# Kernel tuning notes

Measured on AMD Instinct MI355X. Metric: run time of the kernel, lower is better.

## Reference

```python
import jax, jax.numpy as jnp
import numpy as np

N = 8192       # nodes per graph
E = 262144     # edges per graph (avg degree 32)
H = 8          # attention heads
C = 128        # hidden dim per head (H*C = 1024 to match Linear(1024,128))
IN = 128       # input feature dim
NEG_SLOPE = 0.2


def _gat_conv(x, edge_index, W, att_src, att_dst, bias):
    """PyG GATConv (concat=True, add_self_loops=True, shared lin for src/dst)."""
    n = x.shape[0]
    loop = jnp.arange(n, dtype=edge_index.dtype)
    src = jnp.concatenate([edge_index[0], loop])  # [E+N]
    dst = jnp.concatenate([edge_index[1], loop])
    h = (x @ W).reshape(n, H, C)                         # [N,H,C]
    a_src = jnp.sum(h * att_src, axis=-1)                # [N,H]
    a_dst = jnp.sum(h * att_dst, axis=-1)                # [N,H]
    e = jax.nn.leaky_relu(a_src[src] + a_dst[dst], NEG_SLOPE)   # [E+N,H]
    m = jax.ops.segment_max(e, dst, num_segments=n)      # per-dst max for stability
    ex = jnp.exp(e - m[dst])
    den = jax.ops.segment_sum(ex, dst, num_segments=n)
    alpha = ex / den[dst]                                # [E+N,H] neighborhood softmax
    out = jax.ops.segment_sum(h[src] * alpha[:, :, None], dst, num_segments=n)
    return out.reshape(n, H * C) + bias                  # [N, H*C]


def setup_inputs() -> dict:
    key = jax.random.key(0)
    ks = jax.random.split(key, 12)
    s = 0.05  # keep activations in a sane range
    return {
        "x1": jax.random.normal(ks[0], (N, IN), jnp.float32),
        "edge_index1": jax.random.randint(ks[1], (2, E), 0, N, dtype=jnp.int64),
        "W1": jax.random.normal(ks[2], (IN, H * C), jnp.float32) * s,
        "att_src1": jax.random.normal(ks[3], (H, C), jnp.float32) * s,
        "att_dst1": jax.random.normal(ks[4], (H, C), jnp.float32) * s,
        "b1": jnp.zeros((H * C,), jnp.float32),
        "x2": jax.random.normal(ks[5], (N, IN), jnp.float32),
        "edge_index2": jax.random.randint(ks[6], (2, E), 0, N, dtype=jnp.int64),
        "W2": jax.random.normal(ks[7], (IN, H * C), jnp.float32) * s,
        "att_src2": jax.random.normal(ks[8], (H, C), jnp.float32) * s,
        "att_dst2": jax.random.normal(ks[9], (H, C), jnp.float32) * s,
        "b2": jnp.zeros((H * C,), jnp.float32),
        "Wl": jax.random.normal(ks[10], (H * C, 128), jnp.float32) * s,
        "bl": jnp.zeros((128,), jnp.float32),
    }


def reference(x1, edge_index1, W1, att_src1, att_dst1, b1,
              x2, edge_index2, W2, att_src2, att_dst2, b2, Wl, bl):
    emb1 = _gat_conv(x1, edge_index1, W1, att_src1, att_dst1, b1)  # [N1,1024]
    emb2 = _gat_conv(x2, edge_index2, W2, att_src2, att_dst2, b2)  # [N2,1024]
    scores = emb1 @ emb2.T                                          # [N1,N2]
    w1 = jax.nn.softmax(scores, axis=1)
    w2 = jax.nn.softmax(scores, axis=0)
    cross1 = (w2 @ emb2) @ Wl + bl      # [N1,128]
    cross2 = (w1.T @ emb1) @ Wl + bl    # [N2,128]
    return (jnp.mean(cross1, axis=0), jnp.mean(cross2, axis=0))
```

## Files before the change

### kernel.cpp

```cpp
#include <hip/hip_runtime.h>


#define NN 8192
#define EE 262144
#define NEG 0.2f

#define BKT 128
#define RNG (NN / BKT)
#define CAP 2560
#define EB  128
#define CHK (EE / EB)

#define U_CNT   0
#define U_G     (U_CNT + 4*BKT)
#define U_MEMB  (U_G + 2048)
#define U_ZEND  (U_MEMB + 2048)
#define U_U     (U_ZEND)
#define U_ASRC  (U_U + 2*2048)
#define U_ADST  (U_ASRC + 2*NN*8)
#define U_PR    (U_ADST + 2*NN*8)
#define U_WACC  (U_PR + 2*NN*16)
#define U_BIND  (U_WACC + 2*NN*8)
#define U_BINS  (U_BIND + 2*BKT*CAP)
#define ZERO_BYTES ((size_t)U_ZEND * 4)

__global__ __launch_bounds__(256) void k_u(
    const float* __restrict__ W1, const float* __restrict__ as1, const float* __restrict__ ad1,
    const float* __restrict__ W2, const float* __restrict__ as2, const float* __restrict__ ad2,
    float* __restrict__ u) {
  int b = blockIdx.x;
  int graph = b >> 4, sd = (b >> 3) & 1, head = b & 7;
  const float* W = graph ? W2 : W1;
  const float* att = graph ? (sd ? ad2 : as2) : (sd ? ad1 : as1);
  int w = threadIdx.x >> 6, lane = threadIdx.x & 63;
  float2 av = ((const float2*)(att + head * 128))[lane];
  float* uo = u + graph * 2048 + sd * 1024 + head * 128;
#pragma unroll 4
  for (int k = w; k < 128; k += 4) {
    float2 wv = ((const float2*)(W + (size_t)k * 1024 + head * 128))[lane];
    float p = av.x * wv.x + av.y * wv.y;
    p += __shfl_xor(p, 1);  p += __shfl_xor(p, 2);  p += __shfl_xor(p, 4);
    p += __shfl_xor(p, 8);  p += __shfl_xor(p, 16); p += __shfl_xor(p, 32);
    if (lane == 0) uo[k] = p;
  }
}

__global__ __launch_bounds__(256) void k_a(
    const float* __restrict__ x1, const float* __restrict__ x2,
    const float* __restrict__ u, float* __restrict__ asrc, float* __restrict__ adst) {
  int graph = blockIdx.y;
  const float* x = graph ? x2 : x1;
  const float* ug = u + graph * 2048;
  __shared__ float xs[64][129];
  __shared__ float us[16][128];
  int t = threadIdx.x;
  for (int i = t; i < 2048; i += 256) us[i >> 7][i & 127] = ug[i];
  int n0 = blockIdx.x * 64;
  const float* xb = x + (size_t)n0 * 128;
  for (int i = t; i < 64 * 128; i += 256) xs[i >> 7][i & 127] = xb[i];
  __syncthreads();
  int nl = t & 63;
  int j0 = (t >> 6) * 4;
  float a0 = 0.f, a1 = 0.f, a2 = 0.f, a3 = 0.f;
#pragma unroll 4
  for (int k = 0; k < 128; ++k) {
    float xv = xs[nl][k];
    a0 += xv * us[j0 + 0][k];
    a1 += xv * us[j0 + 1][k];
    a2 += xv * us[j0 + 2][k];
    a3 += xv * us[j0 + 3][k];
  }
  int n = n0 + nl;
  float* outp = (j0 < 8) ? (asrc + graph * (NN * 8) + n * 8 + j0)
                         : (adst + graph * (NN * 8) + n * 8 + (j0 - 8));
  outp[0] = a0; outp[1] = a1; outp[2] = a2; outp[3] = a3;
}

__global__ __launch_bounds__(512) void k_bin(
    const int* __restrict__ ei1, const int* __restrict__ ei2,
    int* __restrict__ cnt, int* __restrict__ binD, int* __restrict__ binS) {
  int g = blockIdx.y;
  const int* ei = g ? ei2 : ei1;
  __shared__ int hD[BKT], hS[BKT], scD[BKT], scS[BKT];
  __shared__ int cD[BKT], cS[BKT], bD[BKT], bS[BKT];
  __shared__ int ldsD[CHK], ldsS[CHK];
  __shared__ unsigned char kbAD[CHK], kbAS[CHK];
  int t = threadIdx.x;
  if (t < BKT) { hD[t] = 0; cD[t] = 0; }
  else if (t < 2 * BKT) { int i = t - BKT; hS[i] = 0; cS[i] = 0; }
  __syncthreads();
  int e0 = blockIdx.x * CHK;
  int sv[4], dv[4];
#pragma unroll
  for (int k = 0; k < 4; ++k) {
    sv[k] = ei[e0 + t + k * 512];
    dv[k] = ei[EE + e0 + t + k * 512];
    atomicAdd(&hD[dv[k] >> 6], 1);
    atomicAdd(&hS[sv[k] >> 6], 1);
  }
  __syncthreads();
  if (t < BKT) { scD[t] = hD[t]; bD[t] = atomicAdd(cnt + (2 * g + 0) * BKT + t, hD[t]); }
  else if (t < 2 * BKT) { int i = t - BKT; scS[i] = hS[i]; bS[i] = atomicAdd(cnt + (2 * g + 1) * BKT + i, hS[i]); }
  __syncthreads();
  for (int o = 1; o < BKT; o <<= 1) {
    int v = 0;
    if (t < BKT) { if (t >= o) v = scD[t - o]; }
    else if (t < 2 * BKT) { int i = t - BKT; if (i >= o) v = scS[i - o]; }
    __syncthreads();
    if (t < BKT) scD[t] += v;
    else if (t < 2 * BKT) scS[t - BKT] += v;
    __syncthreads();
  }
#pragma unroll
  for (int k = 0; k < 4; ++k) {
    int kb = dv[k] >> 6;
    int pos = (scD[kb] - hD[kb]) + atomicAdd(&cD[kb], 1);
    ldsD[pos] = (sv[k] << 6) | (dv[k] & 63);
    kbAD[pos] = (unsigned char)kb;
    kb = sv[k] >> 6;
    pos = (scS[kb] - hS[kb]) + atomicAdd(&cS[kb], 1);
    ldsS[pos] = (dv[k] << 6) | (sv[k] & 63);
    kbAS[pos] = (unsigned char)kb;
  }
  __syncthreads();
  int* bdg = binD + (size_t)g * BKT * CAP;
  int* bsg = binS + (size_t)g * BKT * CAP;
#pragma unroll
  for (int k = 0; k < 4; ++k) {
    int i = t + k * 512;
    int kb = kbAD[i];
    bdg[kb * CAP + bD[kb] + (i - (scD[kb] - hD[kb]))] = ldsD[i];
    kb = kbAS[i];
    bsg[kb * CAP + bS[kb] + (i - (scS[kb] - hS[kb]))] = ldsS[i];
  }
}

__global__ __launch_bounds__(512) void k_den_red(
    const int* __restrict__ cnt, const int* __restrict__ binD,
    const float* __restrict__ asrc, const float* __restrict__ adst,
    float* __restrict__ pr) {
  int g = blockIdx.y, b = blockIdx.x;
  int lo = b * RNG;
  const float* as = asrc + g * (NN * 8);
  const float* ad = adst + g * (NN * 8);
  float2* prg = (float2*)pr + (size_t)g * (NN * 8);
  __shared__ float den[8][RNG];
  __shared__ float adsts[8][RNG];
  int t = threadIdx.x;
  {
    int dl = t & 63, h = t >> 6;
    float avv = ad[(lo + dl) * 8 + h];
    float v = as[(lo + dl) * 8 + h] + avv;
    v = v > 0.f ? v : NEG * v;
    adsts[h][dl] = avv;
    den[h][dl] = __expf(v);
  }
  __syncthreads();
  int n = cnt[(2 * g + 0) * BKT + b];
  const int* recs = binD + (size_t)g * BKT * CAP + b * CAP;
  for (int base = 0; base < n; base += 2048) {
    int rv[4]; bool ok[4]; float4 q0[4], q1[4];
#pragma unroll
    for (int k = 0; k < 4; ++k) {
      int i = base + k * 512 + t;
      ok[k] = i < n;
      rv[k] = ok[k] ? recs[i] : 0;
    }
#pragma unroll
    for (int k = 0; k < 4; ++k) {
      const float4* p = (const float4*)(as + (size_t)(rv[k] >> 6) * 8);
      if (ok[k]) { q0[k] = p[0]; q1[k] = p[1]; }
    }
#pragma unroll
    for (int k = 0; k < 4; ++k) {
      if (ok[k]) {
        int dl = rv[k] & 63;
        float e[8] = {q0[k].x, q0[k].y, q0[k].z, q0[k].w,
                      q1[k].x, q1[k].y, q1[k].z, q1[k].w};
#pragma unroll
        for (int h = 0; h < 8; ++h) {
          float v = e[h] + adsts[h][dl];
          v = v > 0.f ? v : NEG * v;
          atomicAdd(&den[h][dl], __expf(v));
        }
      }
    }
  }
  __syncthreads();
  {
    int dl = t >> 3, h = t & 7;
    prg[lo * 8 + t] = make_float2(adsts[h][dl], 1.0f / den[h][dl]);
  }
}

__global__ __launch_bounds__(512) void k_wacc_red(
    const int* __restrict__ cnt, const int* __restrict__ binS,
    const float* __restrict__ asrc, const float* __restrict__ pr,
    float* __restrict__ wacc) {
  int g = blockIdx.y, b = blockIdx.x;
  int lo = b * RNG;
  const float* as = asrc + g * (NN * 8);
  const float2* prg = (const float2*)pr + (size_t)g * (NN * 8);
  __shared__ float wv[8][RNG];
  __shared__ float asrcs[8][RNG];
  int t = threadIdx.x;
  {
    int sl = t & 63, h = t >> 6;
    float sva = as[(lo + sl) * 8 + h];
    float2 f2 = prg[(lo + sl) * 8 + h];
    float v = sva + f2.x;
    v = v > 0.f ? v : NEG * v;
    asrcs[h][sl] = sva;
    wv[h][sl] = __expf(v) * f2.y;
  }
  __syncthreads();
  int n = cnt[(2 * g + 1) * BKT + b];
  const int* recs = binS + (size_t)g * BKT * CAP + b * CAP;
  for (int base = 0; base < n; base += 2048) {
    int rv[4]; bool ok[4]; float4 q0[4], q1[4], q2[4], q3[4];
#pragma unroll
    for (int k = 0; k < 4; ++k) {
      int i = base + k * 512 + t;
      ok[k] = i < n;
      rv[k] = ok[k] ? recs[i] : 0;
    }
#pragma unroll
    for (int k = 0; k < 4; ++k) {
      const float4* p = (const float4*)(prg + (size_t)(rv[k] >> 6) * 8);
      if (ok[k]) { q0[k] = p[0]; q1[k] = p[1]; q2[k] = p[2]; q3[k] = p[3]; }
    }
#pragma unroll
    for (int k = 0; k < 4; ++k) {
      if (ok[k]) {
        int sl = rv[k] & 63;
        float a[8] = {q0[k].x, q0[k].z, q1[k].x, q1[k].z,
                      q2[k].x, q2[k].z, q3[k].x, q3[k].z};
        float r[8] = {q0[k].y, q0[k].w, q1[k].y, q1[k].w,
                      q2[k].y, q2[k].w, q3[k].y, q3[k].w};
#pragma unroll
        for (int h = 0; h < 8; ++h) {
          float v = asrcs[h][sl] + a[h];
          v = v > 0.f ? v : NEG * v;
          atomicAdd(&wv[h][sl], __expf(v) * r[h]);
        }
      }
    }
  }
  __syncthreads();
  {
    int sl = t >> 3, h = t & 7;
    wacc[g * (NN * 8) + lo * 8 + t] = wv[h][sl];
  }
}

#define GCHUNK 256
__global__ __launch_bounds__(256) void k_gred(
    const float* __restrict__ x1, const float* __restrict__ x2,
    const float* __restrict__ wacc, float* __restrict__ g) {
  int graph = blockIdx.y;
  const float* x = graph ? x2 : x1;
  const float* w = wacc + graph * (NN * 8);
  float* gg = g + graph * 1024;
  int t = threadIdx.x;
  int k = t & 127;
  int h0 = (t >> 7) * 4;
  int n0 = blockIdx.x * GCHUNK;
  float a0 = 0.f, a1 = 0.f, a2 = 0.f, a3 = 0.f;
#pragma unroll 4
  for (int n = n0; n < n0 + GCHUNK; ++n) {
    float xv = x[(size_t)n * 128 + k];
    float4 wv4 = *(const float4*)(w + (size_t)n * 8 + h0);
    a0 += xv * wv4.x; a1 += xv * wv4.y; a2 += xv * wv4.z; a3 += xv * wv4.w;
  }
  atomicAdd(gg + (h0 + 0) * 128 + k, a0);
  atomicAdd(gg + (h0 + 1) * 128 + k, a1);
  atomicAdd(gg + (h0 + 2) * 128 + k, a2);
  atomicAdd(gg + (h0 + 3) * 128 + k, a3);
}

__global__ __launch_bounds__(256) void k_memb(
    const float* __restrict__ W1, const float* __restrict__ W2,
    const float* __restrict__ b1, const float* __restrict__ b2,
    const float* __restrict__ g, float* __restrict__ memb) {
  int graph = blockIdx.z;
  int kc = blockIdx.y;
  const float* W = graph ? W2 : W1;
  const float* b = graph ? b2 : b1;
  int e = blockIdx.x * 256 + threadIdx.x;
  int head = e >> 7;
  const float* gr = g + graph * 1024 + head * 128;
  float s = 0.f;
#pragma unroll
  for (int k = kc * 16; k < kc * 16 + 16; ++k) s += gr[k] * W[(size_t)k * 1024 + e];
  s *= (1.0f / (float)NN);
  if (kc == 0) s += b[e];
  atomicAdd(memb + graph * 1024 + e, s);
}

__global__ __launch_bounds__(256) void k_out(
    const float* __restrict__ memb, const float* __restrict__ Wl,
    const float* __restrict__ bl, float* __restrict__ out) {
  int t = threadIdx.x;
  int j = t & 127;
  int k0 = blockIdx.x * 32;
  const float* m = (t < 128) ? (memb + 1024) : memb;
  float s = 0.f;
#pragma unroll
  for (int k = k0; k < k0 + 32; ++k) s += m[k] * Wl[(size_t)k * 128 + j];
  if (blockIdx.x == 0) s += bl[j];
  atomicAdd(out + t, s);
}

extern "C" void kernel_launch(void* const* d_in, const int* in_sizes, int n_in,
                              void* d_out, int out_size, void* d_ws, size_t ws_size,
                              hipStream_t stream) {
  const float* x1  = (const float*)d_in[0];
  const int*   ei1 = (const int*)d_in[1];
  const float* W1  = (const float*)d_in[2];
  const float* as1 = (const float*)d_in[3];
  const float* ad1 = (const float*)d_in[4];
  const float* b1  = (const float*)d_in[5];
  const float* x2  = (const float*)d_in[6];
  const int*   ei2 = (const int*)d_in[7];
  const float* W2  = (const float*)d_in[8];
  const float* as2 = (const float*)d_in[9];
  const float* ad2 = (const float*)d_in[10];
  const float* b2  = (const float*)d_in[11];
  const float* Wl  = (const float*)d_in[12];
  const float* bl  = (const float*)d_in[13];
  float* out = (float*)d_out;

  int*   cnt  = (int*)d_ws + U_CNT;
  float* g    = (float*)d_ws + U_G;
  float* memb = (float*)d_ws + U_MEMB;
  float* u    = (float*)d_ws + U_U;
  float* asrc = (float*)d_ws + U_ASRC;
  float* adst = (float*)d_ws + U_ADST;
  float* pr   = (float*)d_ws + U_PR;
  float* wacc = (float*)d_ws + U_WACC;
  int*   binD = (int*)d_ws + U_BIND;
  int*   binS = (int*)d_ws + U_BINS;

  hipMemsetAsync(d_ws, 0, ZERO_BYTES, stream);
  hipMemsetAsync(d_out, 0, (size_t)out_size * 4, stream);

  k_bin<<<dim3(EB, 2), 512, 0, stream>>>(ei1, ei2, cnt, binD, binS);
  k_u<<<32, 256, 0, stream>>>(W1, as1, ad1, W2, as2, ad2, u);
  k_a<<<dim3(NN / 64, 2), 256, 0, stream>>>(x1, x2, u, asrc, adst);
  k_den_red<<<dim3(BKT, 2), 512, 0, stream>>>(cnt, binD, asrc, adst, pr);
  k_wacc_red<<<dim3(BKT, 2), 512, 0, stream>>>(cnt, binS, asrc, pr, wacc);
  k_gred<<<dim3(NN / GCHUNK, 2), 256, 0, stream>>>(x1, x2, wacc, g);
  k_memb<<<dim3(4, 8, 2), 256, 0, stream>>>(W1, W2, b1, b2, g, memb);
  k_out<<<32, 256, 0, stream>>>(memb, Wl, bl, out);
}
```

Measured before the change: 202.2 us.

## Fuse all stages into one persistent kernel with grid-wide barriers

```diff
diff --git a/kernel.cpp b/kernel.cpp
--- a/kernel.cpp
+++ b/kernel.cpp
@@ -4,311 +4,318 @@
 #define NN 8192
 #define EE 262144
 #define NEG 0.2f
-
 #define BKT 128
-#define RNG (NN / BKT)
+#define RNG 64
 #define CAP 2560
-#define EB  128
-#define CHK (EE / EB)
-
-#define U_CNT   0
-#define U_G     (U_CNT + 4*BKT)
-#define U_MEMB  (U_G + 2048)
-#define U_ZEND  (U_MEMB + 2048)
-#define U_U     (U_ZEND)
-#define U_ASRC  (U_U + 2*2048)
-#define U_ADST  (U_ASRC + 2*NN*8)
-#define U_PR    (U_ADST + 2*NN*8)
-#define U_WACC  (U_PR + 2*NN*16)
-#define U_BIND  (U_WACC + 2*NN*8)
-#define U_BINS  (U_BIND + 2*BKT*CAP)
+#define CHK 2048
+#define GRID 256
+
+#define U_BAR  0
+#define U_CNT  1
+#define U_ZEND (U_CNT + 4*BKT)
+#define U_U    1024
+#define U_ASRC (U_U + 4096)
+#define U_ADST (U_ASRC + 131072)
+#define U_PR   (U_ADST + 131072)
+#define U_WACC (U_PR + 262144)
+#define U_GP   (U_WACC + 131072)
+#define U_GG   (U_GP + 262144)
+#define U_MEMB (U_GG + 2048)
+#define U_BIND (U_MEMB + 2048)
+#define U_BINS (U_BIND + 2*BKT*CAP)
 #define ZERO_BYTES ((size_t)U_ZEND * 4)
 
-__global__ __launch_bounds__(256) void k_u(
-    const float* __restrict__ W1, const float* __restrict__ as1, const float* __restrict__ ad1,
-    const float* __restrict__ W2, const float* __restrict__ as2, const float* __restrict__ ad2,
-    float* __restrict__ u) {
-  int b = blockIdx.x;
-  int graph = b >> 4, sd = (b >> 3) & 1, head = b & 7;
-  const float* W = graph ? W2 : W1;
-  const float* att = graph ? (sd ? ad2 : as2) : (sd ? ad1 : as1);
-  int w = threadIdx.x >> 6, lane = threadIdx.x & 63;
-  float2 av = ((const float2*)(att + head * 128))[lane];
-  float* uo = u + graph * 2048 + sd * 1024 + head * 128;
+__device__ __forceinline__ void gbar(int* bar, int target) {
+  __syncthreads();
+  if (threadIdx.x == 0) {
+    __threadfence();
+    atomicAdd(bar, 1);
+    while (atomicAdd(bar, 0) < target) {
+      __builtin_amdgcn_s_sleep(2);
+    }
+    __threadfence();
+  }
+  __syncthreads();
+}
+
+__global__ __launch_bounds__(512, 2) void k_mega(
+    const float* __restrict__ x1, const int* __restrict__ ei1,
+    const float* __restrict__ W1, const float* __restrict__ as1,
+    const float* __restrict__ ad1, const float* __restrict__ b1,
+    const float* __restrict__ x2, const int* __restrict__ ei2,
+    const float* __restrict__ W2, const float* __restrict__ as2,
+    const float* __restrict__ ad2, const float* __restrict__ b2,
+    const float* __restrict__ Wl, const float* __restrict__ bl,
+    float* __restrict__ out, int* __restrict__ ws_i, float* __restrict__ ws_f) {
+  int* bar   = ws_i + U_BAR;
+  int* cnt   = ws_i + U_CNT;
+  float* uu  = ws_f + U_U;
+  float* asrc = ws_f + U_ASRC;
+  float* adst = ws_f + U_ADST;
+  float* pr   = ws_f + U_PR;
+  float* wacc = ws_f + U_WACC;
+  float* gpart = ws_f + U_GP;
+  float* gg   = ws_f + U_GG;
+  float* memb = ws_f + U_MEMB;
+  int* binD  = ws_i + U_BIND;
+  int* binS  = ws_i + U_BINS;
+
+  __shared__ union {
+    struct {
+      int hD[BKT], hS[BKT], scD[BKT], scS[BKT];
+      int cD[BKT], cS[BKT], bD[BKT], bS[BKT];
+      int ldsD[CHK], ldsS[CHK];
+      unsigned char kbAD[CHK], kbAS[CHK];
+    } bin;
+    struct { float xs[64][129]; float us[16][128]; } a;
+    struct { float den[RNG * 8]; float adsts[RNG * 8]; } dr;
+    struct { float wv[RNG * 8]; float asrcs[RNG * 8]; } wr;
+    float red[512];
+  } sm;
+
+  int t = threadIdx.x;
+
+  {
+    int unit = blockIdx.x, g = unit >> 7, chunk = unit & 127;
+    const int* ei = g ? ei2 : ei1;
+    if (t < BKT) { sm.bin.hD[t] = 0; sm.bin.cD[t] = 0; }
+    else if (t < 2 * BKT) { int i = t - BKT; sm.bin.hS[i] = 0; sm.bin.cS[i] = 0; }
+    __syncthreads();
+    int e0 = chunk * CHK;
+    int sv[4], dv[4];
+#pragma unroll
+    for (int k = 0; k < 4; ++k) {
+      sv[k] = ei[e0 + t + k * 512];
+      dv[k] = ei[EE + e0 + t + k * 512];
+      atomicAdd(&sm.bin.hD[dv[k] >> 6], 1);
+      atomicAdd(&sm.bin.hS[sv[k] >> 6], 1);
+    }
+    __syncthreads();
+    if (t < BKT) { sm.bin.scD[t] = sm.bin.hD[t]; sm.bin.bD[t] = atomicAdd(cnt + (2 * g + 0) * BKT + t, sm.bin.hD[t]); }
+    else if (t < 2 * BKT) { int i = t - BKT; sm.bin.scS[i] = sm.bin.hS[i]; sm.bin.bS[i] = atomicAdd(cnt + (2 * g + 1) * BKT + i, sm.bin.hS[i]); }
+    __syncthreads();
+    for (int o = 1; o < BKT; o <<= 1) {
+      int v = 0;
+      if (t < BKT) { if (t >= o) v = sm.bin.scD[t - o]; }
+      else if (t < 2 * BKT) { int i = t - BKT; if (i >= o) v = sm.bin.scS[i - o]; }
+      __syncthreads();
+      if (t < BKT) sm.bin.scD[t] += v;
+      else if (t < 2 * BKT) sm.bin.scS[t - BKT] += v;
+      __syncthreads();
+    }
+#pragma unroll
+    for (int k = 0; k < 4; ++k) {
+      int kb = dv[k] >> 6;
+      int pos = (sm.bin.scD[kb] - sm.bin.hD[kb]) + atomicAdd(&sm.bin.cD[kb], 1);
+      sm.bin.ldsD[pos] = (sv[k] << 6) | (dv[k] & 63);
+      sm.bin.kbAD[pos] = (unsigned char)kb;
+      kb = sv[k] >> 6;
+      pos = (sm.bin.scS[kb] - sm.bin.hS[kb]) + atomicAdd(&sm.bin.cS[kb], 1);
+      sm.bin.ldsS[pos] = (dv[k] << 6) | (sv[k] & 63);
+      sm.bin.kbAS[pos] = (unsigned char)kb;
+    }
+    __syncthreads();
+    int* bdg = binD + (size_t)g * BKT * CAP;
+    int* bsg = binS + (size_t)g * BKT * CAP;
+#pragma unroll
+    for (int k = 0; k < 4; ++k) {
+      int i = t + k * 512;
+      int kb = sm.bin.kbAD[i];
+      bdg[kb * CAP + sm.bin.bD[kb] + (i - (sm.bin.scD[kb] - sm.bin.hD[kb]))] = sm.bin.ldsD[i];
+      kb = sm.bin.kbAS[i];
+      bsg[kb * CAP + sm.bin.bS[kb] + (i - (sm.bin.scS[kb] - sm.bin.hS[kb]))] = sm.bin.ldsS[i];
+    }
+    if (blockIdx.x < 32 && t < 128) {
+      int g2 = blockIdx.x >> 4, sd = (blockIdx.x >> 3) & 1, head = blockIdx.x & 7;
+      const float* W = g2 ? W2 : W1;
+      const float* att = g2 ? (sd ? ad2 : as2) : (sd ? ad1 : as1);
+      const float* wr2 = W + (size_t)t * 1024 + head * 128;
+      const float* ar = att + head * 128;
+      float s = 0.f;
+#pragma unroll 8
+      for (int c = 0; c < 128; ++c) s += wr2[c] * ar[c];
+      uu[g2 * 2048 + sd * 1024 + head * 128 + t] = s;
+    }
+  }
+  gbar(bar, GRID * 1);
+
+  {
+    int unit = blockIdx.x, g = unit >> 7, tile = unit & 127;
+    const float* x = g ? x2 : x1;
+    const float* ug = uu + g * 2048;
+    for (int i = t; i < 2048; i += 512) sm.a.us[i >> 7][i & 127] = ug[i];
+    int n0 = tile * 64;
+    const float* xb = x + (size_t)n0 * 128;
+    for (int i = t; i < 64 * 128; i += 512) sm.a.xs[i >> 7][i & 127] = xb[i];
+    __syncthreads();
+    int nl = t & 63, j0 = (t >> 6) * 2;
+    float a0 = 0.f, a1 = 0.f;
 #pragma unroll 4
-  for (int k = w; k < 128; k += 4) {
-    float2 wv = ((const float2*)(W + (size_t)k * 1024 + head * 128))[lane];
-    float p = av.x * wv.x + av.y * wv.y;
-    p += __shfl_xor(p, 1);  p += __shfl_xor(p, 2);  p += __shfl_xor(p, 4);
-    p += __shfl_xor(p, 8);  p += __shfl_xor(p, 16); p += __shfl_xor(p, 32);
-    if (lane == 0) uo[k] = p;
-  }
-}
-
-__global__ __launch_bounds__(256) void k_a(
-    const float* __restrict__ x1, const float* __restrict__ x2,
-    const float* __restrict__ u, float* __restrict__ asrc, float* __restrict__ adst) {
-  int graph = blockIdx.y;
-  const float* x = graph ? x2 : x1;
-  const float* ug = u + graph * 2048;
-  __shared__ float xs[64][129];
-  __shared__ float us[16][128];
-  int t = threadIdx.x;
-  for (int i = t; i < 2048; i += 256) us[i >> 7][i & 127] = ug[i];
-  int n0 = blockIdx.x * 64;
-  const float* xb = x + (size_t)n0 * 128;
-  for (int i = t; i < 64 * 128; i += 256) xs[i >> 7][i & 127] = xb[i];
-  __syncthreads();
-  int nl = t & 63;
-  int j0 = (t >> 6) * 4;
-  float a0 = 0.f, a1 = 0.f, a2 = 0.f, a3 = 0.f;
-#pragma unroll 4
-  for (int k = 0; k < 128; ++k) {
-    float xv = xs[nl][k];
-    a0 += xv * us[j0 + 0][k];
-    a1 += xv * us[j0 + 1][k];
-    a2 += xv * us[j0 + 2][k];
-    a3 += xv * us[j0 + 3][k];
-  }
-  int n = n0 + nl;
-  float* outp = (j0 < 8) ? (asrc + graph * (NN * 8) + n * 8 + j0)
-                         : (adst + graph * (NN * 8) + n * 8 + (j0 - 8));
-  outp[0] = a0; outp[1] = a1; outp[2] = a2; outp[3] = a3;
-}
-
-__global__ __launch_bounds__(512) void k_bin(
-    const int* __restrict__ ei1, const int* __restrict__ ei2,
-    int* __restrict__ cnt, int* __restrict__ binD, int* __restrict__ binS) {
-  int g = blockIdx.y;
-  const int* ei = g ? ei2 : ei1;
-  __shared__ int hD[BKT], hS[BKT], scD[BKT], scS[BKT];
-  __shared__ int cD[BKT], cS[BKT], bD[BKT], bS[BKT];
-  __shared__ int ldsD[CHK], ldsS[CHK];
-  __shared__ unsigned char kbAD[CHK], kbAS[CHK];
-  int t = threadIdx.x;
-  if (t < BKT) { hD[t] = 0; cD[t] = 0; }
-  else if (t < 2 * BKT) { int i = t - BKT; hS[i] = 0; cS[i] = 0; }
-  __syncthreads();
-  int e0 = blockIdx.x * CHK;
-  int sv[4], dv[4];
-#pragma unroll
-  for (int k = 0; k < 4; ++k) {
-    sv[k] = ei[e0 + t + k * 512];
-    dv[k] = ei[EE + e0 + t + k * 512];
-    atomicAdd(&hD[dv[k] >> 6], 1);
-    atomicAdd(&hS[sv[k] >> 6], 1);
-  }
-  __syncthreads();
-  if (t < BKT) { scD[t] = hD[t]; bD[t] = atomicAdd(cnt + (2 * g + 0) * BKT + t, hD[t]); }
-  else if (t < 2 * BKT) { int i = t - BKT; scS[i] = hS[i]; bS[i] = atomicAdd(cnt + (2 * g + 1) * BKT + i, hS[i]); }
-  __syncthreads();
-  for (int o = 1; o < BKT; o <<= 1) {
-    int v = 0;
-    if (t < BKT) { if (t >= o) v = scD[t - o]; }
-    else if (t < 2 * BKT) { int i = t - BKT; if (i >= o) v = scS[i - o]; }
-    __syncthreads();
-    if (t < BKT) scD[t] += v;
-    else if (t < 2 * BKT) scS[t - BKT] += v;
-    __syncthreads();
-  }
-#pragma unroll
-  for (int k = 0; k < 4; ++k) {
-    int kb = dv[k] >> 6;
-    int pos = (scD[kb] - hD[kb]) + atomicAdd(&cD[kb], 1);
-    ldsD[pos] = (sv[k] << 6) | (dv[k] & 63);
-    kbAD[pos] = (unsigned char)kb;
-    kb = sv[k] >> 6;
-    pos = (scS[kb] - hS[kb]) + atomicAdd(&cS[kb], 1);
-    ldsS[pos] = (dv[k] << 6) | (sv[k] & 63);
-    kbAS[pos] = (unsigned char)kb;
-  }
-  __syncthreads();
-  int* bdg = binD + (size_t)g * BKT * CAP;
-  int* bsg = binS + (size_t)g * BKT * CAP;
-#pragma unroll
-  for (int k = 0; k < 4; ++k) {
-    int i = t + k * 512;
-    int kb = kbAD[i];
-    bdg[kb * CAP + bD[kb] + (i - (scD[kb] - hD[kb]))] = ldsD[i];
-    kb = kbAS[i];
-    bsg[kb * CAP + bS[kb] + (i - (scS[kb] - hS[kb]))] = ldsS[i];
-  }
-}
-
-__global__ __launch_bounds__(512) void k_den_red(
-    const int* __restrict__ cnt, const int* __restrict__ binD,
-    const float* __restrict__ asrc, const float* __restrict__ adst,
-    float* __restrict__ pr) {
-  int g = blockIdx.y, b = blockIdx.x;
-  int lo = b * RNG;
-  const float* as = asrc + g * (NN * 8);
-  const float* ad = adst + g * (NN * 8);
-  float2* prg = (float2*)pr + (size_t)g * (NN * 8);
-  __shared__ float den[8][RNG];
-  __shared__ float adsts[8][RNG];
-  int t = threadIdx.x;
-  {
-    int dl = t & 63, h = t >> 6;
-    float avv = ad[(lo + dl) * 8 + h];
-    float v = as[(lo + dl) * 8 + h] + avv;
-    v = v > 0.f ? v : NEG * v;
-    adsts[h][dl] = avv;
-    den[h][dl] = __expf(v);
-  }
-  __syncthreads();
-  int n = cnt[(2 * g + 0) * BKT + b];
-  const int* recs = binD + (size_t)g * BKT * CAP + b * CAP;
-  for (int base = 0; base < n; base += 2048) {
-    int rv[4]; bool ok[4]; float4 q0[4], q1[4];
-#pragma unroll
-    for (int k = 0; k < 4; ++k) {
-      int i = base + k * 512 + t;
-      ok[k] = i < n;
-      rv[k] = ok[k] ? recs[i] : 0;
-    }
-#pragma unroll
-    for (int k = 0; k < 4; ++k) {
-      const float4* p = (const float4*)(as + (size_t)(rv[k] >> 6) * 8);
-      if (ok[k]) { q0[k] = p[0]; q1[k] = p[1]; }
-    }
-#pragma unroll
-    for (int k = 0; k < 4; ++k) {
-      if (ok[k]) {
-        int dl = rv[k] & 63;
-        float e[8] = {q0[k].x, q0[k].y, q0[k].z, q0[k].w,
-                      q1[k].x, q1[k].y, q1[k].z, q1[k].w};
-#pragma unroll
-        for (int h = 0; h < 8; ++h) {
-          float v = e[h] + adsts[h][dl];
+    for (int k = 0; k < 128; ++k) {
+      float xv = sm.a.xs[nl][k];
+      a0 += xv * sm.a.us[j0][k];
+      a1 += xv * sm.a.us[j0 + 1][k];
+    }
+    int n = n0 + nl;
+    float* outp = (j0 < 8) ? (asrc + g * (NN * 8) + n * 8 + j0)
+                           : (adst + g * (NN * 8) + n * 8 + (j0 - 8));
+    outp[0] = a0; outp[1] = a1;
+  }
+  gbar(bar, GRID * 2);
+
+  {
+    int unit = blockIdx.x, g = unit >> 7, b = unit & 127;
+    int lo = b * RNG;
+    const float* as_ = asrc + g * (NN * 8);
+    const float* ad_ = adst + g * (NN * 8);
+    float2* prg = (float2*)pr + (size_t)g * (NN * 8);
+    for (int i = t; i < RNG * 8; i += 512) {
+      float avv = ad_[lo * 8 + i];
+      float v = as_[lo * 8 + i] + avv;
+      v = v > 0.f ? v : NEG * v;
+      sm.dr.adsts[i] = avv;
+      sm.dr.den[i] = __expf(v);
+    }
+    __syncthreads();
+    int n = cnt[(2 * g + 0) * BKT + b];
+    const int* recs = binD + (size_t)g * BKT * CAP + b * CAP;
+    int rid = t >> 3, h = t & 7;
+    for (int base = 0; base < n; base += 256) {
+      int rv[4]; bool ok[4]; float svv[4];
+#pragma unroll
+      for (int k = 0; k < 4; ++k) {
+        int i = base + k * 64 + rid;
+        ok[k] = i < n;
+        rv[k] = ok[k] ? recs[i] : 0;
+      }
+#pragma unroll
+      for (int k = 0; k < 4; ++k) svv[k] = ok[k] ? as_[(rv[k] >> 6) * 8 + h] : 0.f;
+#pragma unroll
+      for (int k = 0; k < 4; ++k) {
+        if (ok[k]) {
+          int dl = rv[k] & 63;
+          float v = svv[k] + sm.dr.adsts[dl * 8 + h];
           v = v > 0.f ? v : NEG * v;
-          atomicAdd(&den[h][dl], __expf(v));
+          atomicAdd(&sm.dr.den[dl * 8 + h], __expf(v));
         }
       }
     }
-  }
-  __syncthreads();
-  {
-    int dl = t >> 3, h = t & 7;
-    prg[lo * 8 + t] = make_float2(adsts[h][dl], 1.0f / den[h][dl]);
-  }
-}
-
-__global__ __launch_bounds__(512) void k_wacc_red(
-    const int* __restrict__ cnt, const int* __restrict__ binS,
-    const float* __restrict__ asrc, const float* __restrict__ pr,
-    float* __restrict__ wacc) {
-  int g = blockIdx.y, b = blockIdx.x;
-  int lo = b * RNG;
-  const float* as = asrc + g * (NN * 8);
-  const float2* prg = (const float2*)pr + (size_t)g * (NN * 8);
-  __shared__ float wv[8][RNG];
-  __shared__ float asrcs[8][RNG];
-  int t = threadIdx.x;
-  {
-    int sl = t & 63, h = t >> 6;
-    float sva = as[(lo + sl) * 8 + h];
-    float2 f2 = prg[(lo + sl) * 8 + h];
-    float v = sva + f2.x;
-    v = v > 0.f ? v : NEG * v;
-    asrcs[h][sl] = sva;
-    wv[h][sl] = __expf(v) * f2.y;
-  }
-  __syncthreads();
-  int n = cnt[(2 * g + 1) * BKT + b];
-  const int* recs = binS + (size_t)g * BKT * CAP + b * CAP;
-  for (int base = 0; base < n; base += 2048) {
-    int rv[4]; bool ok[4]; float4 q0[4], q1[4], q2[4], q3[4];
-#pragma unroll
-    for (int k = 0; k < 4; ++k) {
-      int i = base + k * 512 + t;
-      ok[k] = i < n;
-      rv[k] = ok[k] ? recs[i] : 0;
-    }
-#pragma unroll
-    for (int k = 0; k < 4; ++k) {
-      const float4* p = (const float4*)(prg + (size_t)(rv[k] >> 6) * 8);
-      if (ok[k]) { q0[k] = p[0]; q1[k] = p[1]; q2[k] = p[2]; q3[k] = p[3]; }
-    }
-#pragma unroll
-    for (int k = 0; k < 4; ++k) {
-      if (ok[k]) {
-        int sl = rv[k] & 63;
-        float a[8] = {q0[k].x, q0[k].z, q1[k].x, q1[k].z,
-                      q2[k].x, q2[k].z, q3[k].x, q3[k].z};
-        float r[8] = {q0[k].y, q0[k].w, q1[k].y, q1[k].w,
-                      q2[k].y, q2[k].w, q3[k].y, q3[k].w};
-#pragma unroll
-        for (int h = 0; h < 8; ++h) {
-          float v = asrcs[h][sl] + a[h];
+    __syncthreads();
+    for (int i = t; i < RNG * 8; i += 512)
+      prg[lo * 8 + i] = make_float2(sm.dr.adsts[i], 1.0f / sm.dr.den[i]);
+  }
+  gbar(bar, GRID * 3);
+
+  {
+    int unit = blockIdx.x, g = unit >> 7, b = unit & 127;
+    int lo = b * RNG;
+    const float* as_ = asrc + g * (NN * 8);
+    const float2* prg = (const float2*)pr + (size_t)g * (NN * 8);
+    for (int i = t; i < RNG * 8; i += 512) {
+      float sva = as_[lo * 8 + i];
+      float2 f2 = prg[lo * 8 + i];
+      float v = sva + f2.x;
+      v = v > 0.f ? v : NEG * v;
+      sm.wr.asrcs[i] = sva;
+      sm.wr.wv[i] = __expf(v) * f2.y;
+    }
+    __syncthreads();
+    int n = cnt[(2 * g + 1) * BKT + b];
+    const int* recs = binS + (size_t)g * BKT * CAP + b * CAP;
+    int rid = t >> 3, h = t & 7;
+    for (int base = 0; base < n; base += 256) {
+      int rv[4]; bool ok[4]; float2 pv[4];
+#pragma unroll
+      for (int k = 0; k < 4; ++k) {
+        int i = base + k * 64 + rid;
+        ok[k] = i < n;
+        rv[k] = ok[k] ? recs[i] : 0;
+      }
+#pragma unroll
+      for (int k = 0; k < 4; ++k)
+        pv[k] = ok[k] ? prg[(size_t)(rv[k] >> 6) * 8 + h] : make_float2(0.f, 0.f);
+#pragma unroll
+      for (int k = 0; k < 4; ++k) {
+        if (ok[k]) {
+          int sl = rv[k] & 63;
+          float v = sm.wr.asrcs[sl * 8 + h] + pv[k].x;
           v = v > 0.f ? v : NEG * v;
-          atomicAdd(&wv[h][sl], __expf(v) * r[h]);
+          atomicAdd(&sm.wr.wv[sl * 8 + h], __expf(v) * pv[k].y);
         }
       }
     }
-  }
-  __syncthreads();
-  {
-    int sl = t >> 3, h = t & 7;
-    wacc[g * (NN * 8) + lo * 8 + t] = wv[h][sl];
-  }
-}
-
-#define GCHUNK 256
-__global__ __launch_bounds__(256) void k_gred(
-    const float* __restrict__ x1, const float* __restrict__ x2,
-    const float* __restrict__ wacc, float* __restrict__ g) {
-  int graph = blockIdx.y;
-  const float* x = graph ? x2 : x1;
-  const float* w = wacc + graph * (NN * 8);
-  float* gg = g + graph * 1024;
-  int t = threadIdx.x;
-  int k = t & 127;
-  int h0 = (t >> 7) * 4;
-  int n0 = blockIdx.x * GCHUNK;
-  float a0 = 0.f, a1 = 0.f, a2 = 0.f, a3 = 0.f;
+    __syncthreads();
+    for (int i = t; i < RNG * 8; i += 512)
+      wacc[g * (NN * 8) + lo * 8 + i] = sm.wr.wv[i];
+  }
+  gbar(bar, GRID * 4);
+
+  {
+    int unit = blockIdx.x, g = unit >> 7, chunk = unit & 127;
+    int n0 = chunk * 64;
+    const float* x = g ? x2 : x1;
+    const float* w = wacc + g * (NN * 8);
+    int k = t & 127, h0 = (t >> 7) * 2;
+    float a0 = 0.f, a1 = 0.f;
 #pragma unroll 4
-  for (int n = n0; n < n0 + GCHUNK; ++n) {
-    float xv = x[(size_t)n * 128 + k];
-    float4 wv4 = *(const float4*)(w + (size_t)n * 8 + h0);
-    a0 += xv * wv4.x; a1 += xv * wv4.y; a2 += xv * wv4.z; a3 += xv * wv4.w;
-  }
-  atomicAdd(gg + (h0 + 0) * 128 + k, a0);
-  atomicAdd(gg + (h0 + 1) * 128 + k, a1);
-  atomicAdd(gg + (h0 + 2) * 128 + k, a2);
-  atomicAdd(gg + (h0 + 3) * 128 + k, a3);
-}
-
-__global__ __launch_bounds__(256) void k_memb(
-    const float* __restrict__ W1, const float* __restrict__ W2,
-    const float* __restrict__ b1, const float* __restrict__ b2,
-    const float* __restrict__ g, float* __restrict__ memb) {
-  int graph = blockIdx.z;
-  int kc = blockIdx.y;
-  const float* W = graph ? W2 : W1;
-  const float* b = graph ? b2 : b1;
-  int e = blockIdx.x * 256 + threadIdx.x;
-  int head = e >> 7;
-  const float* gr = g + graph * 1024 + head * 128;
-  float s = 0.f;
-#pragma unroll
-  for (int k = kc * 16; k < kc * 16 + 16; ++k) s += gr[k] * W[(size_t)k * 1024 + e];
-  s *= (1.0f / (float)NN);
-  if (kc == 0) s += b[e];
-  atomicAdd(memb + graph * 1024 + e, s);
-}
-
-__global__ __launch_bounds__(256) void k_out(
-    const float* __restrict__ memb, const float* __restrict__ Wl,
-    const float* __restrict__ bl, float* __restrict__ out) {
-  int t = threadIdx.x;
-  int j = t & 127;
-  int k0 = blockIdx.x * 32;
-  const float* m = (t < 128) ? (memb + 1024) : memb;
-  float s = 0.f;
-#pragma unroll
-  for (int k = k0; k < k0 + 32; ++k) s += m[k] * Wl[(size_t)k * 128 + j];
-  if (blockIdx.x == 0) s += bl[j];
-  atomicAdd(out + t, s);
+    for (int n = n0; n < n0 + 64; ++n) {
+      float xv = x[(size_t)n * 128 + k];
+      float2 w2 = *(const float2*)(w + (size_t)n * 8 + h0);
+      a0 += xv * w2.x; a1 += xv * w2.y;
+    }
+    float* gp = gpart + (size_t)unit * 1024;
+    gp[h0 * 128 + k] = a0;
+    gp[(h0 + 1) * 128 + k] = a1;
+  }
+  gbar(bar, GRID * 5);
+
+  {
+    int e0 = blockIdx.x * 8;
+    int g = e0 >> 10, idx = e0 & 1023;
+    const float* gp = gpart + (size_t)(g * 128) * 1024;
+    int c = t >> 3, eoff = t & 7;
+    float v = gp[(size_t)c * 1024 + idx + eoff] + gp[(size_t)(c + 64) * 1024 + idx + eoff];
+    sm.red[t] = v;
+    __syncthreads();
+    for (int cs = 32; cs >= 1; cs >>= 1) {
+      if (t < cs * 8) sm.red[t] += sm.red[t + cs * 8];
+      __syncthreads();
+    }
+    if (t < 8) gg[e0 + t] = sm.red[t];
+  }
+  gbar(bar, GRID * 6);
+
+  {
+    int e0 = blockIdx.x * 8;
+    int g = e0 >> 10, e1024 = e0 & 1023, head = e1024 >> 7;
+    const float* W = g ? W2 : W1;
+    const float* bb = g ? b2 : b1;
+    const float* gr = gg + g * 1024 + head * 128;
+    int k2 = t >> 3, eoff = t & 7;
+    float v = gr[k2] * W[(size_t)k2 * 1024 + e1024 + eoff]
+            + gr[k2 + 64] * W[(size_t)(k2 + 64) * 1024 + e1024 + eoff];
+    sm.red[t] = v;
+    __syncthreads();
+    for (int cs = 32; cs >= 1; cs >>= 1) {
+      if (t < cs * 8) sm.red[t] += sm.red[t + cs * 8];
+      __syncthreads();
+    }
+    if (t < 8) memb[e0 + t] = sm.red[t] * (1.0f / (float)NN) + bb[e1024 + t];
+  }
+  gbar(bar, GRID * 7);
+
+  {
+    int b = blockIdx.x, j = b & 127;
+    const float* m = (b < 128) ? (memb + 1024) : memb;
+    float v = m[t] * Wl[(size_t)t * 128 + j] + m[t + 512] * Wl[(size_t)(t + 512) * 128 + j];
+    sm.red[t] = v;
+    __syncthreads();
+    for (int s = 256; s >= 1; s >>= 1) {
+      if (t < s) sm.red[t] += sm.red[t + s];
+      __syncthreads();
+    }
+    if (t == 0) out[b] = sm.red[0] + bl[j];
+  }
 }
 
 extern "C" void kernel_launch(void* const* d_in, const int* in_sizes, int n_in,
@@ -328,28 +335,11 @@
   const float* b2  = (const float*)d_in[11];
   const float* Wl  = (const float*)d_in[12];
   const float* bl  = (const float*)d_in[13];
-  float* out = (float*)d_out;
-
-  int*   cnt  = (int*)d_ws + U_CNT;
-  float* g    = (float*)d_ws + U_G;
-  float* memb = (float*)d_ws + U_MEMB;
-  float* u    = (float*)d_ws + U_U;
-  float* asrc = (float*)d_ws + U_ASRC;
-  float* adst = (float*)d_ws + U_ADST;
-  float* pr   = (float*)d_ws + U_PR;
-  float* wacc = (float*)d_ws + U_WACC;
-  int*   binD = (int*)d_ws + U_BIND;
-  int*   binS = (int*)d_ws + U_BINS;
 
   hipMemsetAsync(d_ws, 0, ZERO_BYTES, stream);
-  hipMemsetAsync(d_out, 0, (size_t)out_size * 4, stream);
-
-  k_bin<<<dim3(EB, 2), 512, 0, stream>>>(ei1, ei2, cnt, binD, binS);
-  k_u<<<32, 256, 0, stream>>>(W1, as1, ad1, W2, as2, ad2, u);
-  k_a<<<dim3(NN / 64, 2), 256, 0, stream>>>(x1, x2, u, asrc, adst);
-  k_den_red<<<dim3(BKT, 2), 512, 0, stream>>>(cnt, binD, asrc, adst, pr);
-  k_wacc_red<<<dim3(BKT, 2), 512, 0, stream>>>(cnt, binS, asrc, pr, wacc);
-  k_gred<<<dim3(NN / GCHUNK, 2), 256, 0, stream>>>(x1, x2, wacc, g);
-  k_memb<<<dim3(4, 8, 2), 256, 0, stream>>>(W1, W2, b1, b2, g, memb);
-  k_out<<<32, 256, 0, stream>>>(memb, Wl, bl, out);
+
+  k_mega<<<GRID, 512, 0, stream>>>(x1, ei1, W1, as1, ad1, b1,
+                                   x2, ei2, W2, as2, ad2, b2,
+                                   Wl, bl, (float*)d_out,
+                                   (int*)d_ws, (float*)d_ws);
 }
```

New measurement: 307.6 us. +52.1%, slower.
